# Performance work log

Measured on AMD Instinct MI355X. Metric: run time of the kernel, lower is better.

## Reference

```python
import jax, jax.numpy as jnp
import numpy as np

NUM_HEADS = 8
NEG_INF = -2**32 + 1  # matches the TF code's masking constant


def setup_inputs() -> dict:
    key = jax.random.key(0)
    ks = jax.random.split(key, 12)
    B, L, D_IN, D_MODEL = 2, 2048, 256, 256
    s = 1.0 / np.sqrt(D_IN)
    return {
        "queries": jax.random.normal(ks[0], (B, L, D_IN), jnp.float32),
        "keys": jax.random.normal(ks[1], (B, L, D_IN), jnp.float32),
        "values": jax.random.normal(ks[2], (B, L, D_IN), jnp.float32),
        "key_mask": jax.random.randint(ks[3], (B, L, 1), 0, 2, jnp.int32),
        "Wq": jax.random.normal(ks[4], (D_IN, D_MODEL), jnp.float32) * s,
        "bq": jnp.zeros((D_MODEL,), jnp.float32),
        "Wk": jax.random.normal(ks[5], (D_IN, D_MODEL), jnp.float32) * s,
        "bk": jnp.zeros((D_MODEL,), jnp.float32),
        "Wv": jax.random.normal(ks[6], (D_IN, D_MODEL), jnp.float32) * s,
        "bv": jnp.zeros((D_MODEL,), jnp.float32),
        "Wo": jax.random.normal(ks[7], (D_MODEL, D_IN), jnp.float32) * s,
        "bo": jnp.zeros((D_IN,), jnp.float32),
    }


def reference(queries, keys, values, key_mask, Wq, bq, Wk, bk, Wv, bv, Wo, bo):
    B, Lq, _ = queries.shape
    Lk = keys.shape[1]
    h = NUM_HEADS
    d_model = Wq.shape[1]
    depth = d_model // h

    Q = queries @ Wq + bq  # [B, Lq, d_model]
    K = keys @ Wk + bk     # [B, Lk, d_model]
    V = values @ Wv + bv   # [B, Lk, d_model]

    # split heads: contiguous chunks of size depth along feature dim
    Qh = Q.reshape(B, Lq, h, depth)
    Kh = K.reshape(B, Lk, h, depth)
    Vh = V.reshape(B, Lk, h, depth)

    scores = jnp.einsum("bqhd,bkhd->bhqk", Qh, Kh) / jnp.sqrt(
        jnp.asarray(depth, jnp.float32)
    )  # [B, h, Lq, Lk]

    # key_mask: [B, Lk, 1] -> broadcast over heads and query positions
    mask = (key_mask[:, None, :, 0] != 0)[:, :, None, :]  # [B, 1, 1, Lk]
    scores = jnp.where(mask, scores, jnp.asarray(NEG_INF, scores.dtype))

    attn = jax.nn.softmax(scores, axis=-1)  # dropout is identity at inference
    out = jnp.einsum("bhqk,bkhd->bqhd", attn, Vh).reshape(B, Lq, d_model)
    return out @ Wo + bo  # [B, Lq, input_dim]
```

## Files before the change

kernel.cpp:

```cpp
#include <hip/hip_runtime.h>

#define Bn 2
#define Ln 2048
#define DIN 256
#define Hn 8
#define DEPTH 32
#define SCALE 0.17677669529663687f
#define NEGC (-4294967296.0f)
#define WLS 264

typedef _Float16 f16;
typedef _Float16 h8 __attribute__((ext_vector_type(8)));
typedef _Float16 h4 __attribute__((ext_vector_type(4)));
typedef float f4 __attribute__((ext_vector_type(4)));


__global__ __launch_bounds__(256) void projKV(
    const float* __restrict__ Xk, const float* __restrict__ Xv,
    const float* __restrict__ Wk, const float* __restrict__ Wv,
    const float* __restrict__ bk, const float* __restrict__ bv,
    f16* S, int b)
{
    __shared__ f16 Wl[64 * WLS];
    const int p = blockIdx.z;
    const float* X = (p ? Xv : Xk) + (size_t)b * Ln * DIN;
    const float* W = p ? Wv : Wk;
    const float* bias = p ? bv : bk;

    const int t = threadIdx.x, w = t >> 6, lane = t & 63;
    const int l15 = lane & 15, quad = lane >> 4;
    const int n0 = blockIdx.y * 64;

    {
        const int nl = t & 63, kb = t >> 6;
        for (int kk = 0; kk < 64; ++kk) {
            const int k = kk * 4 + kb;
            Wl[nl * WLS + k] = (f16)W[(size_t)k * DIN + n0 + nl];
        }
    }
    __syncthreads();

    const int m0w = blockIdx.x * 128 + w * 32;
    const float* A0 = X + (size_t)(m0w + l15) * DIN;
    const float* A1 = X + (size_t)(m0w + 16 + l15) * DIN;

    f4 acc[2][4];
    #pragma unroll
    for (int mi = 0; mi < 2; ++mi)
        #pragma unroll
        for (int tt = 0; tt < 4; ++tt) acc[mi][tt] = (f4){0.f, 0.f, 0.f, 0.f};

    for (int k0 = 0; k0 < DIN; k0 += 32) {
        float4 xa0 = *(const float4*)(A0 + k0 + quad * 8);
        float4 xb0 = *(const float4*)(A0 + k0 + quad * 8 + 4);
        float4 xa1 = *(const float4*)(A1 + k0 + quad * 8);
        float4 xb1 = *(const float4*)(A1 + k0 + quad * 8 + 4);
        h8 af0 = { (f16)xa0.x, (f16)xa0.y, (f16)xa0.z, (f16)xa0.w,
                   (f16)xb0.x, (f16)xb0.y, (f16)xb0.z, (f16)xb0.w };
        h8 af1 = { (f16)xa1.x, (f16)xa1.y, (f16)xa1.z, (f16)xa1.w,
                   (f16)xb1.x, (f16)xb1.y, (f16)xb1.z, (f16)xb1.w };
        #pragma unroll
        for (int tt = 0; tt < 4; ++tt) {
            h8 bf = *(const h8*)(Wl + (tt * 16 + l15) * WLS + k0 + quad * 8);
            acc[0][tt] = __builtin_amdgcn_mfma_f32_16x16x32_f16(af0, bf, acc[0][tt], 0, 0, 0);
            acc[1][tt] = __builtin_amdgcn_mfma_f32_16x16x32_f16(af1, bf, acc[1][tt], 0, 0, 0);
        }
    }
    #pragma unroll
    for (int mi = 0; mi < 2; ++mi)
        #pragma unroll
        for (int tt = 0; tt < 4; ++tt) {
            const int c = n0 + tt * 16 + l15;
            const float bb = bias[c];
            const int h = c >> 5, dd = c & 31;
            #pragma unroll
            for (int r = 0; r < 4; ++r) {
                const int l = m0w + mi * 16 + quad * 4 + r;
                const float v = acc[mi][tt][r] + bb;
                const unsigned hg = (unsigned)h * 128 + (l >> 4);
                unsigned j;
                if (!p)
                    j = (hg * 64 + (unsigned)(dd >> 3) * 16 + (l & 15)) * 8 + (dd & 7);
                else
                    j = 524288u + ((hg * 2 + (dd >> 4)) * 64
                        + (unsigned)((l & 15) >> 2) * 16 + (dd & 15)) * 4 + (l & 3);
                S[(((size_t)(j >> 12)) << 13) + 4096u + (j & 4095u)] = (f16)v;
            }
        }
}

__global__ __launch_bounds__(512) void flashQ(
    const float* __restrict__ Xq, const float* __restrict__ Wq,
    const float* __restrict__ bq, const int* __restrict__ mask,
    float* outbuf, int b)
{
    __shared__ union {
        struct { f16 Wlq[32 * WLS]; f16 Qs[2048]; } a;
        struct { float Os[8][32][68]; float lS[8][64]; } c;
    } sm;
    f16* S = (f16*)outbuf;
    const int t = threadIdx.x, w = t >> 6, lane = t & 63;
    const int l15 = lane & 15, quad = lane >> 4;
    const int h = blockIdx.x, q0 = blockIdx.y * 64;

    {
        const int nl = t & 31, kb = t >> 5;
        for (int kk = 0; kk < 16; ++kk) {
            const int k = kk * 16 + kb;
            sm.a.Wlq[nl * WLS + k] = (f16)Wq[(size_t)k * DIN + h * 32 + nl];
        }
    }
    __syncthreads();

    if (w < 4) {
        const float* A0 = Xq + (size_t)(b * Ln + q0 + w * 16 + l15) * DIN;
        f4 a2[2] = { {0.f,0.f,0.f,0.f}, {0.f,0.f,0.f,0.f} };
        #pragma unroll
        for (int kk = 0; kk < 8; ++kk) {
            const int k0 = kk * 32;
            float4 xa = *(const float4*)(A0 + k0 + quad * 8);
            float4 xb = *(const float4*)(A0 + k0 + quad * 8 + 4);
            h8 af = { (f16)xa.x, (f16)xa.y, (f16)xa.z, (f16)xa.w,
                      (f16)xb.x, (f16)xb.y, (f16)xb.z, (f16)xb.w };
            #pragma unroll
            for (int tt = 0; tt < 2; ++tt) {
                h8 bf = *(const h8*)(sm.a.Wlq + (tt * 16 + l15) * WLS + k0 + quad * 8);
                a2[tt] = __builtin_amdgcn_mfma_f32_16x16x32_f16(af, bf, a2[tt], 0, 0, 0);
            }
        }
        #pragma unroll
        for (int tt = 0; tt < 2; ++tt) {
            const int c = tt * 16 + l15;
            const float bb = bq[h * 32 + c];
            #pragma unroll
            for (int r = 0; r < 4; ++r) {
                const int lc = quad * 4 + r;
                sm.a.Qs[((size_t)w * 64 + (c >> 3) * 16 + lc) * 8 + (c & 7)] =
                    (f16)((a2[tt][r] + bb) * SCALE);
            }
        }
    }
    __syncthreads();
    h8 qf[4];
    #pragma unroll
    for (int qg = 0; qg < 4; ++qg)
        qf[qg] = *(const h8*)(sm.a.Qs + ((size_t)qg * 64 + lane) * 8);
    __syncthreads();

    const int* mrow = mask + b * Ln;

    f4 o[2][4];
    #pragma unroll
    for (int i = 0; i < 2; ++i)
        #pragma unroll
        for (int j = 0; j < 4; ++j) o[i][j] = (f4){0.f, 0.f, 0.f, 0.f};
    float l_run[4] = {0.f, 0.f, 0.f, 0.f};
    const int k_base = w * (Ln / 8);

    for (int kt = 0; kt < Ln / 8 / 64; ++kt) {
        const int k0 = k_base + kt * 64;
        #pragma unroll
        for (int tt = 0; tt < 4; ++tt) {
            const int g = (k0 >> 4) + tt;
            const size_t kaddr = ((size_t)(h * 16 + (g >> 3)) << 13) + 4096u
                               + (size_t)((g & 7) * 512 + lane * 8);
            h8 kf = *(const h8*)(S + kaddr);
            const int4 mk = *(const int4*)(mrow + g * 16 + quad * 4);
            f4 bias4 = { mk.x ? 0.f : NEGC, mk.y ? 0.f : NEGC,
                         mk.z ? 0.f : NEGC, mk.w ? 0.f : NEGC };
            const size_t vaddr = ((size_t)(128 + h * 16 + (g >> 3)) << 13) + 4096u
                               + (size_t)((g & 7) * 512 + lane * 4);
            h4 va0 = *(const h4*)(S + vaddr);
            h4 va1 = *(const h4*)(S + vaddr + 256);
            f4 s_[4];
            #pragma unroll
            for (int qg = 0; qg < 4; ++qg)
                s_[qg] = __builtin_amdgcn_mfma_f32_16x16x32_f16(kf, qf[qg], bias4, 0, 0, 0);
            #pragma unroll
            for (int qg = 0; qg < 4; ++qg) {
                h4 pf;
                #pragma unroll
                for (int r = 0; r < 4; ++r) {
                    const float pv = __expf(s_[qg][r]);
                    l_run[qg] += pv;
                    pf[r] = (f16)pv;
                }
                o[0][qg] = __builtin_amdgcn_mfma_f32_16x16x16f16(va0, pf, o[0][qg], 0, 0, 0);
                o[1][qg] = __builtin_amdgcn_mfma_f32_16x16x16f16(va1, pf, o[1][qg], 0, 0, 0);
            }
        }
    }
    #pragma unroll
    for (int qg = 0; qg < 4; ++qg) {
        l_run[qg] += __shfl_xor(l_run[qg], 16, 64);
        l_run[qg] += __shfl_xor(l_run[qg], 32, 64);
        if (quad == 0) sm.c.lS[w][qg * 16 + l15] = l_run[qg];
        #pragma unroll
        for (int dg = 0; dg < 2; ++dg)
            #pragma unroll
            for (int r = 0; r < 4; ++r)
                sm.c.Os[w][dg * 16 + quad * 4 + r][qg * 16 + l15] = o[dg][qg][r];
    }
    __syncthreads();

    if (t < 256) {
        const int cq = t & 63, dv = t >> 6;
        float ls = 0.f;
        #pragma unroll
        for (int i = 0; i < 8; ++i) ls += sm.c.lS[i][cq];
        const float inv = 1.0f / ls;
        h8 pack;
        #pragma unroll
        for (int i = 0; i < 8; ++i) {
            const int dd = dv * 8 + i;
            float ov = 0.f;
            #pragma unroll
            for (int s = 0; s < 8; ++s) ov += sm.c.Os[s][dd][cq];
            pack[i] = (f16)(ov * inv);
        }
        const int gm = b * 128 + ((q0 + cq) >> 4);
        *(h8*)(S + (size_t)gm * 8192
               + (size_t)(h * 64 + dv * 16 + (cq & 15)) * 8) = pack;
    }
}

__global__ __launch_bounds__(256) void outproj(
    const float* __restrict__ Wo, const float* __restrict__ bo, float* outbuf)
{
    f16* S = (f16*)outbuf;
    const int t = threadIdx.x, w = t >> 6, lane = t & 63;
    const int l15 = lane & 15, quad = lane >> 4;
    const int g = blockIdx.x;

    h8 af[8];
    #pragma unroll
    for (int h = 0; h < 8; ++h)
        af[h] = *(const h8*)(S + (size_t)g * 8192 + (size_t)(h * 64 + lane) * 8);
    __syncthreads();

    const float* Wop = Wo + w * 64 + l15;
    f4 acc[4] = {{0.f,0.f,0.f,0.f},{0.f,0.f,0.f,0.f},
                 {0.f,0.f,0.f,0.f},{0.f,0.f,0.f,0.f}};
    #pragma unroll
    for (int h = 0; h < 8; ++h) {
        h8 bf[4];
        #pragma unroll
        for (int tt = 0; tt < 4; ++tt)
            #pragma unroll
            for (int j = 0; j < 8; ++j)
                bf[tt][j] = (f16)Wop[(size_t)(h * 32 + quad * 8 + j) * DIN + tt * 16];
        #pragma unroll
        for (int tt = 0; tt < 4; ++tt)
            acc[tt] = __builtin_amdgcn_mfma_f32_16x16x32_f16(af[h], bf[tt], acc[tt], 0, 0, 0);
    }
    #pragma unroll
    for (int tt = 0; tt < 4; ++tt) {
        const int c = w * 64 + tt * 16 + l15;
        const float bb = bo[c];
        #pragma unroll
        for (int r = 0; r < 4; ++r)
            outbuf[(size_t)(g * 16 + quad * 4 + r) * DIN + c] = acc[tt][r] + bb;
    }
}

extern "C" void kernel_launch(void* const* d_in, const int* in_sizes, int n_in,
                              void* d_out, int out_size, void* d_ws, size_t ws_size,
                              hipStream_t stream) {
    (void)in_sizes; (void)n_in; (void)d_ws; (void)ws_size; (void)out_size;
    const float* Xq = (const float*)d_in[0];
    const float* Xk = (const float*)d_in[1];
    const float* Xv = (const float*)d_in[2];
    const int*  mask = (const int*)d_in[3];
    const float* Wq = (const float*)d_in[4];
    const float* bq = (const float*)d_in[5];
    const float* Wk = (const float*)d_in[6];
    const float* bk = (const float*)d_in[7];
    const float* Wv = (const float*)d_in[8];
    const float* bv = (const float*)d_in[9];
    const float* Wo = (const float*)d_in[10];
    const float* bo = (const float*)d_in[11];
    float* out = (float*)d_out;
    f16* S = (f16*)out;

    projKV<<<dim3(16, 4, 2), 256, 0, stream>>>(Xk, Xv, Wk, Wv, bk, bv, S, 0);
    flashQ<<<dim3(8, 32), 512, 0, stream>>>(Xq, Wq, bq, mask, out, 0);
    projKV<<<dim3(16, 4, 2), 256, 0, stream>>>(Xk, Xv, Wk, Wv, bk, bv, S, 1);
    flashQ<<<dim3(8, 32), 512, 0, stream>>>(Xq, Wq, bq, mask, out, 1);
    outproj<<<256, 256, 0, stream>>>(Wo, bo, out);
}
```

Measured before the change: 140.0 us.

## Use workspace buffers to run Q/K/V projection, attention, and output in three launches

When the workspace is large enough, the code moves intermediates out of the output buffer and into separate Q/K/V/O fp16 workspace buffers. This allows one projection GEMM for Q, K and V across both batches, a single flash-attention launch over all batch-heads with finer query chunks (32 rows, 256 threads), and one output GEMM. It replaces five serialized launches, in which each flash kernel recomputed its Q projection and the batches ran one after another, with three launches and more blocks per launch. The old output-buffer-aliasing path stays as a fallback when the workspace is too small, so behaviour depends on ws_size.

After: 122.4 us. -12.6%, faster.

```diff
diff --git a/kernel.cpp b/kernel.cpp
--- a/kernel.cpp
+++ b/kernel.cpp
@@ -7,6 +7,7 @@
 #define DEPTH 32
 #define SCALE 0.17677669529663687f
 #define NEGC (-4294967296.0f)
+#define NG  (Ln / 16)
 #define WLS 264
 
 typedef _Float16 f16;
@@ -15,7 +16,210 @@
 typedef float f4 __attribute__((ext_vector_type(4)));
 
 
-__global__ __launch_bounds__(256) void projKV(
+__global__ __launch_bounds__(256) void proj_gemm(
+    const float* __restrict__ Xq, const float* __restrict__ Xk, const float* __restrict__ Xv,
+    const float* __restrict__ Wq, const float* __restrict__ Wk, const float* __restrict__ Wv,
+    const float* __restrict__ bq, const float* __restrict__ bk, const float* __restrict__ bv,
+    f16* __restrict__ Qz, f16* __restrict__ Kz, f16* __restrict__ Vz)
+{
+    __shared__ f16 Wl[64 * WLS];
+    const int p = blockIdx.z;
+    const float* X = p == 0 ? Xq : p == 1 ? Xk : Xv;
+    const float* W = p == 0 ? Wq : p == 1 ? Wk : Wv;
+    const float* bias = p == 0 ? bq : p == 1 ? bk : bv;
+
+    const int t = threadIdx.x, w = t >> 6, lane = t & 63;
+    const int l15 = lane & 15, quad = lane >> 4;
+    const int n0 = blockIdx.y * 64;
+
+    {
+        const int nl = t & 63, kb = t >> 6;
+        for (int kk = 0; kk < 64; ++kk) {
+            const int k = kk * 4 + kb;
+            Wl[nl * WLS + k] = (f16)W[(size_t)k * DIN + n0 + nl];
+        }
+    }
+    __syncthreads();
+
+    const int m0w = blockIdx.x * 128 + w * 32;
+    const float* A0 = X + (size_t)(m0w + l15) * DIN;
+    const float* A1 = X + (size_t)(m0w + 16 + l15) * DIN;
+
+    f4 acc[2][4];
+    #pragma unroll
+    for (int mi = 0; mi < 2; ++mi)
+        #pragma unroll
+        for (int tt = 0; tt < 4; ++tt) acc[mi][tt] = (f4){0.f, 0.f, 0.f, 0.f};
+
+    for (int k0 = 0; k0 < DIN; k0 += 32) {
+        float4 xa0 = *(const float4*)(A0 + k0 + quad * 8);
+        float4 xb0 = *(const float4*)(A0 + k0 + quad * 8 + 4);
+        float4 xa1 = *(const float4*)(A1 + k0 + quad * 8);
+        float4 xb1 = *(const float4*)(A1 + k0 + quad * 8 + 4);
+        h8 af0 = { (f16)xa0.x, (f16)xa0.y, (f16)xa0.z, (f16)xa0.w,
+                   (f16)xb0.x, (f16)xb0.y, (f16)xb0.z, (f16)xb0.w };
+        h8 af1 = { (f16)xa1.x, (f16)xa1.y, (f16)xa1.z, (f16)xa1.w,
+                   (f16)xb1.x, (f16)xb1.y, (f16)xb1.z, (f16)xb1.w };
+        #pragma unroll
+        for (int tt = 0; tt < 4; ++tt) {
+            h8 bf = *(const h8*)(Wl + (tt * 16 + l15) * WLS + k0 + quad * 8);
+            acc[0][tt] = __builtin_amdgcn_mfma_f32_16x16x32_f16(af0, bf, acc[0][tt], 0, 0, 0);
+            acc[1][tt] = __builtin_amdgcn_mfma_f32_16x16x32_f16(af1, bf, acc[1][tt], 0, 0, 0);
+        }
+    }
+    #pragma unroll
+    for (int mi = 0; mi < 2; ++mi)
+        #pragma unroll
+        for (int tt = 0; tt < 4; ++tt) {
+            const int c = n0 + tt * 16 + l15;
+            const float bb = bias[c];
+            const int h = c >> 5, dd = c & 31;
+            #pragma unroll
+            for (int r = 0; r < 4; ++r) {
+                const int row = m0w + mi * 16 + quad * 4 + r;
+                const int b = row >> 11, l = row & (Ln - 1);
+                const float v = acc[mi][tt][r] + bb;
+                const size_t hbg = (size_t)(b * Hn + h) * NG + (l >> 4);
+                if (p == 0)
+                    Qz[(hbg * 64 + (dd >> 3) * 16 + (l & 15)) * 8 + (dd & 7)] =
+                        (f16)(v * SCALE);
+                else if (p == 1)
+                    Kz[(hbg * 64 + (dd >> 3) * 16 + (l & 15)) * 8 + (dd & 7)] = (f16)v;
+                else
+                    Vz[((hbg * 2 + (dd >> 4)) * 64 + ((l & 15) >> 2) * 16 + (dd & 15)) * 4
+                       + (l & 3)] = (f16)v;
+            }
+        }
+}
+
+__global__ __launch_bounds__(256) void flash_mfma(
+    const f16* __restrict__ Qz, const f16* __restrict__ Kz,
+    const f16* __restrict__ Vz, const int* __restrict__ mask,
+    f16* __restrict__ Oz)
+{
+    __shared__ float Os[4][32][34];
+    __shared__ float lS[4][32];
+    const int t = threadIdx.x, w = t >> 6, lane = t & 63;
+    const int l15 = lane & 15, quad = lane >> 4;
+    const int qc = blockIdx.x, hb = blockIdx.y;
+    const int q0 = qc * 32;
+    const int b = hb >> 3, h = hb & 7;
+    const f16* Qh = Qz + (size_t)hb * NG * 512;
+    const f16* Kh = Kz + (size_t)hb * NG * 512;
+    const f16* Vh = Vz + (size_t)hb * NG * 512;
+    const int* mrow = mask + b * Ln;
+    const int k_base = w * (Ln / 4);
+
+    h8 qf[2];
+    #pragma unroll
+    for (int qg = 0; qg < 2; ++qg)
+        qf[qg] = *(const h8*)(Qh + ((size_t)(qc * 2 + qg) * 64 + lane) * 8);
+
+    f4 o[2][2];
+    #pragma unroll
+    for (int i = 0; i < 2; ++i)
+        #pragma unroll
+        for (int j = 0; j < 2; ++j) o[i][j] = (f4){0.f, 0.f, 0.f, 0.f};
+    float l_run[2] = {0.f, 0.f};
+
+    for (int kt = 0; kt < Ln / 4 / 64; ++kt) {
+        const int k0 = k_base + kt * 64;
+        #pragma unroll
+        for (int tt = 0; tt < 4; ++tt) {
+            const int g = (k0 >> 4) + tt;
+            h8 kf = *(const h8*)(Kh + ((size_t)g * 64 + lane) * 8);
+            const int4 mk = *(const int4*)(mrow + g * 16 + quad * 4);
+            f4 bias4 = { mk.x ? 0.f : NEGC, mk.y ? 0.f : NEGC,
+                         mk.z ? 0.f : NEGC, mk.w ? 0.f : NEGC };
+            h4 va0 = *(const h4*)(Vh + ((size_t)(g * 2)     * 64 + lane) * 4);
+            h4 va1 = *(const h4*)(Vh + ((size_t)(g * 2 + 1) * 64 + lane) * 4);
+            f4 s[2];
+            #pragma unroll
+            for (int qg = 0; qg < 2; ++qg)
+                s[qg] = __builtin_amdgcn_mfma_f32_16x16x32_f16(kf, qf[qg], bias4, 0, 0, 0);
+            #pragma unroll
+            for (int qg = 0; qg < 2; ++qg) {
+                h4 pf;
+                #pragma unroll
+                for (int r = 0; r < 4; ++r) {
+                    const float pv = __expf(s[qg][r]);
+                    l_run[qg] += pv;
+                    pf[r] = (f16)pv;
+                }
+                o[0][qg] = __builtin_amdgcn_mfma_f32_16x16x16f16(va0, pf, o[0][qg], 0, 0, 0);
+                o[1][qg] = __builtin_amdgcn_mfma_f32_16x16x16f16(va1, pf, o[1][qg], 0, 0, 0);
+            }
+        }
+    }
+    #pragma unroll
+    for (int qg = 0; qg < 2; ++qg) {
+        l_run[qg] += __shfl_xor(l_run[qg], 16, 64);
+        l_run[qg] += __shfl_xor(l_run[qg], 32, 64);
+        if (quad == 0) lS[w][qg * 16 + l15] = l_run[qg];
+        #pragma unroll
+        for (int dg = 0; dg < 2; ++dg)
+            #pragma unroll
+            for (int r = 0; r < 4; ++r)
+                Os[w][dg * 16 + quad * 4 + r][qg * 16 + l15] = o[dg][qg][r];
+    }
+    __syncthreads();
+
+    if (t < 128) {
+        const int cq = t & 31, dv = t >> 5;
+        const float ls = lS[0][cq] + lS[1][cq] + lS[2][cq] + lS[3][cq];
+        const float inv = 1.0f / ls;
+        h8 pack;
+        #pragma unroll
+        for (int i = 0; i < 8; ++i) {
+            const int dd = dv * 8 + i;
+            const float ov = Os[0][dd][cq] + Os[1][dd][cq] +
+                             Os[2][dd][cq] + Os[3][dd][cq];
+            pack[i] = (f16)(ov * inv);
+        }
+        const int gm = b * NG + ((q0 + cq) >> 4);
+        *(h8*)(Oz + (((size_t)gm * 8 + h) * 64 + dv * 16 + (cq & 15)) * 8) = pack;
+    }
+}
+
+__global__ __launch_bounds__(256) void out_gemm(
+    const f16* __restrict__ Oz, const float* __restrict__ Wo,
+    const float* __restrict__ bo, float* __restrict__ out)
+{
+    const int t = threadIdx.x, w = t >> 6, lane = t & 63;
+    const int l15 = lane & 15, quad = lane >> 4;
+    const int g = blockIdx.x;
+
+    h8 af[8];
+    #pragma unroll
+    for (int h = 0; h < 8; ++h)
+        af[h] = *(const h8*)(Oz + (((size_t)g * 8 + h) * 64 + lane) * 8);
+
+    const float* Wop = Wo + w * 64 + l15;
+    f4 acc[4] = {{0.f,0.f,0.f,0.f},{0.f,0.f,0.f,0.f},
+                 {0.f,0.f,0.f,0.f},{0.f,0.f,0.f,0.f}};
+    #pragma unroll
+    for (int h = 0; h < 8; ++h) {
+        h8 bf[4];
+        #pragma unroll
+        for (int tt = 0; tt < 4; ++tt)
+            #pragma unroll
+            for (int j = 0; j < 8; ++j)
+                bf[tt][j] = (f16)Wop[(size_t)(h * 32 + quad * 8 + j) * DIN + tt * 16];
+        #pragma unroll
+        for (int tt = 0; tt < 4; ++tt)
+            acc[tt] = __builtin_amdgcn_mfma_f32_16x16x32_f16(af[h], bf[tt], acc[tt], 0, 0, 0);
+    }
+    #pragma unroll
+    for (int tt = 0; tt < 4; ++tt) {
+        const int c = w * 64 + tt * 16 + l15;
+        const float bb = bo[c];
+        #pragma unroll
+        for (int r = 0; r < 4; ++r)
+            out[(size_t)(g * 16 + quad * 4 + r) * DIN + c] = acc[tt][r] + bb;
+    }
+}
+
+__global__ __launch_bounds__(256) void fb_projKV(
     const float* __restrict__ Xk, const float* __restrict__ Xv,
     const float* __restrict__ Wk, const float* __restrict__ Wv,
     const float* __restrict__ bk, const float* __restrict__ bv,
@@ -89,7 +293,7 @@
         }
 }
 
-__global__ __launch_bounds__(512) void flashQ(
+__global__ __launch_bounds__(512) void fb_flashQ(
     const float* __restrict__ Xq, const float* __restrict__ Wq,
     const float* __restrict__ bq, const int* __restrict__ mask,
     float* outbuf, int b)
@@ -148,7 +352,6 @@
     __syncthreads();
 
     const int* mrow = mask + b * Ln;
-
     f4 o[2][4];
     #pragma unroll
     for (int i = 0; i < 2; ++i)
@@ -224,7 +427,7 @@
     }
 }
 
-__global__ __launch_bounds__(256) void outproj(
+__global__ __launch_bounds__(256) void fb_outproj(
     const float* __restrict__ Wo, const float* __restrict__ bo, float* outbuf)
 {
     f16* S = (f16*)outbuf;
@@ -266,7 +469,7 @@
 extern "C" void kernel_launch(void* const* d_in, const int* in_sizes, int n_in,
                               void* d_out, int out_size, void* d_ws, size_t ws_size,
                               hipStream_t stream) {
-    (void)in_sizes; (void)n_in; (void)d_ws; (void)ws_size; (void)out_size;
+    (void)in_sizes; (void)n_in; (void)out_size;
     const float* Xq = (const float*)d_in[0];
     const float* Xk = (const float*)d_in[1];
     const float* Xv = (const float*)d_in[2];
@@ -280,11 +483,25 @@
     const float* Wo = (const float*)d_in[10];
     const float* bo = (const float*)d_in[11];
     float* out = (float*)d_out;
-    f16* S = (f16*)out;
-
-    projKV<<<dim3(16, 4, 2), 256, 0, stream>>>(Xk, Xv, Wk, Wv, bk, bv, S, 0);
-    flashQ<<<dim3(8, 32), 512, 0, stream>>>(Xq, Wq, bq, mask, out, 0);
-    projKV<<<dim3(16, 4, 2), 256, 0, stream>>>(Xk, Xv, Wk, Wv, bk, bv, S, 1);
-    flashQ<<<dim3(8, 32), 512, 0, stream>>>(Xq, Wq, bq, mask, out, 1);
-    outproj<<<256, 256, 0, stream>>>(Wo, bo, out);
-}
+
+    const size_t HB_E = (size_t)Bn * Hn * Ln * DEPTH;
+    const size_t need = 4 * HB_E * sizeof(f16);
+
+    if (ws_size >= need) {
+        f16* Qz = (f16*)d_ws;
+        f16* Kz = Qz + HB_E;
+        f16* Vz = Kz + HB_E;
+        f16* Oz = Vz + HB_E;
+        proj_gemm<<<dim3(Bn * Ln / 128, DIN / 64, 3), 256, 0, stream>>>(
+            Xq, Xk, Xv, Wq, Wk, Wv, bq, bk, bv, Qz, Kz, Vz);
+        flash_mfma<<<dim3(Ln / 32, Bn * Hn), 256, 0, stream>>>(Qz, Kz, Vz, mask, Oz);
+        out_gemm<<<Bn * Ln / 16, 256, 0, stream>>>(Oz, Wo, bo, out);
+    } else {
+        f16* S = (f16*)out;
+        fb_projKV<<<dim3(16, 4, 2), 256, 0, stream>>>(Xk, Xv, Wk, Wv, bk, bv, S, 0);
+        fb_flashQ<<<dim3(8, 32), 512, 0, stream>>>(Xq, Wq, bq, mask, out, 0);
+        fb_projKV<<<dim3(16, 4, 2), 256, 0, stream>>>(Xk, Xv, Wk, Wv, bk, bv, S, 1);
+        fb_flashQ<<<dim3(8, 32), 512, 0, stream>>>(Xq, Wq, bq, mask, out, 1);
+        fb_outproj<<<256, 256, 0, stream>>>(Wo, bo, out);
+    }
+}
```
